# Kernel optimization log

Measured on AMD Instinct MI355X. Metric: run time of the kernel, lower is better.

The kernel has to match this reference:

```python
import jax, jax.numpy as jnp
import numpy as np

B, N, D, KD = 8, 2048, 64, 64

def setup_inputs() -> dict:
    key = jax.random.key(0)
    ks = jax.random.split(key, 7)
    s = 1.0 / np.sqrt(D)
    return {
        "x":  jax.random.normal(ks[0], (B, N, D), dtype=jnp.float32),
        "Wq": jax.random.normal(ks[1], (D, KD), dtype=jnp.float32) * s,
        "bq": jnp.zeros((KD,), jnp.float32),
        "Wk": jax.random.normal(ks[2], (D, KD), dtype=jnp.float32) * s,
        "bk": jnp.zeros((KD,), jnp.float32),
        "Wv": jax.random.normal(ks[3], (D, KD), dtype=jnp.float32) * s,
        "bv": jnp.zeros((KD,), jnp.float32),
    }

def reference(x, Wq, bq, Wk, bk, Wv, bv):
    # Q,K,V: [B,N,KD]
    Q = x @ Wq + bq
    K = x @ Wk + bk
    V = x @ Wv + bv
    # scores: [B,N,N] (note: original applies NO 1/sqrt(d) scaling)
    scores = jnp.einsum('bij,bkj->bik', Q, K)
    probs = jax.nn.softmax(scores, axis=-1)
    # mean-threshold sparsification: keep entries above the row mean
    mask = (probs > jnp.mean(probs, axis=-1, keepdims=True)).astype(probs.dtype)
    sparse = probs * mask
    out = jnp.einsum('bij,bjk->bik', sparse, V)  # [B,N,KD]
    return out
```

## Files before the change

### kernel.cpp

```cpp
#include <hip/hip_runtime.h>

#define NB 8
#define NS 2048
#define ND 64
#define LOG2E 1.44269504f

typedef _Float16 half8 __attribute__((ext_vector_type(8)));
typedef __attribute__((ext_vector_type(4))) float floatx4;

__device__ __forceinline__ half8 cvt8(const float* p) {
    float4 a = *(const float4*)p;
    float4 b = *(const float4*)(p + 4);
    half8 h = {(_Float16)a.x, (_Float16)a.y, (_Float16)a.z, (_Float16)a.w,
               (_Float16)b.x, (_Float16)b.y, (_Float16)b.z, (_Float16)b.w};
    return h;
}
__device__ __forceinline__ half8 cvtWcol(const float* base) {
    half8 h;
#pragma unroll
    for (int j = 0; j < 8; ++j) h[j] = (_Float16)base[j * 64];
    return h;
}

__global__ __launch_bounds__(256) void qkv_proj(
    const float* __restrict__ x,
    const float* __restrict__ Wq, const float* __restrict__ bq,
    const float* __restrict__ Wk, const float* __restrict__ bk,
    const float* __restrict__ Wv, const float* __restrict__ bv,
    _Float16* __restrict__ Qg, _Float16* __restrict__ Kg,
    _Float16* __restrict__ Vt)
{
    __shared__ _Float16 vt[64 * 18];

    const int tid  = threadIdx.x;
    const int wv   = tid >> 6;
    const int l    = tid & 63;
    const int quad = l >> 4;
    const int tx   = l & 15;

    const int b  = blockIdx.x & 7;
    const int n0 = (blockIdx.x >> 3) * 16;

    const float* xr = x + ((size_t)b * NS + n0 + tx) * ND + quad * 8;
    half8 a0 = cvt8(xr);
    half8 a1 = cvt8(xr + 32);

    const floatx4 zf = {0.f, 0.f, 0.f, 0.f};

#pragma unroll
    for (int i = 0; i < 3; ++i) {
        const int ct = wv * 3 + i;
        const int m  = ct >> 2;
        const int lcol = (ct & 3) * 16 + tx;

        const float* Wm;
        const float* Bm;
        if (m == 0)      { Wm = Wq; Bm = bq; }
        else if (m == 1) { Wm = Wk; Bm = bk; }
        else             { Wm = Wv; Bm = bv; }

        half8 b0 = cvtWcol(Wm + (quad * 8) * 64 + lcol);
        half8 b1 = cvtWcol(Wm + (32 + quad * 8) * 64 + lcol);

        floatx4 acc = __builtin_amdgcn_mfma_f32_16x16x32_f16(a0, b0, zf, 0, 0, 0);
        acc = __builtin_amdgcn_mfma_f32_16x16x32_f16(a1, b1, acc, 0, 0, 0);
        const float bias = Bm[lcol];

        if (m == 0) {
#pragma unroll
            for (int r = 0; r < 4; ++r)
                Qg[((size_t)b * NS + n0 + quad * 4 + r) * ND + lcol] =
                    (_Float16)((acc[r] + bias) * LOG2E);
        } else if (m == 1) {
#pragma unroll
            for (int r = 0; r < 4; ++r)
                Kg[((size_t)b * NS + n0 + quad * 4 + r) * ND + lcol] = (_Float16)(acc[r] + bias);
        } else {
#pragma unroll
            for (int r = 0; r < 4; ++r)
                vt[lcol * 18 + quad * 4 + r] = (_Float16)(acc[r] + bias);
        }
    }
    __syncthreads();
    {
        const int d = tid >> 2, seg = tid & 3;
        uint2 p = *(uint2*)&vt[d * 18 + seg * 4];
        *(uint2*)(Vt + ((size_t)b * ND + d) * NS + n0 + seg * 4) = p;
    }
}

__global__ __launch_bounds__(512, 4) void attn(
    const _Float16* __restrict__ Qg,
    const _Float16* __restrict__ Kg,
    const _Float16* __restrict__ Vt,
    float* __restrict__ out)
{
    __shared__ __align__(16) unsigned char smraw[8 * 2 * 16 * 76 * 2];
    __shared__ float lsh[128];
    _Float16* pbuf = (_Float16*)smraw;
    float*    obuf = (float*)smraw;

    const int tid  = threadIdx.x;
    const int wv   = tid >> 6;
    const int l    = tid & 63;
    const int quad = l >> 4;
    const int tx   = l & 15;

    const int b  = blockIdx.x & 7;
    const int q0 = (blockIdx.x >> 3) * 16;

    const _Float16* Qb = Qg + ((size_t)b * NS + q0) * ND;
    const _Float16* Kb = Kg + (size_t)b * NS * ND;
    const _Float16* Vb = Vt + (size_t)b * ND * NS;

    half8 qf0 = *(const half8*)(Qb + (size_t)tx * ND + quad * 8);
    half8 qf1 = *(const half8*)(Qb + (size_t)tx * ND + 32 + quad * 8);

    const floatx4 zf = {0.f, 0.f, 0.f, 0.f};

#define KROW(s) ((((s) >> 2) * 8 + wv) * 64 + ((s) & 3) * 16 + tx)

    floatx4 e[4][4];
    float lacc[4] = {0.f, 0.f, 0.f, 0.f};
    {
        half8 kf[6][2];
#pragma unroll
        for (int s = 0; s < 6; ++s) {
            const _Float16* Kr = Kb + (size_t)KROW(s) * ND + quad * 8;
            kf[s][0] = *(const half8*)Kr;
            kf[s][1] = *(const half8*)(Kr + 32);
        }
#pragma unroll
        for (int s = 0; s < 16; ++s) {
            floatx4 c = __builtin_amdgcn_mfma_f32_16x16x32_f16(qf0, kf[s % 6][0], zf, 0, 0, 0);
            c = __builtin_amdgcn_mfma_f32_16x16x32_f16(qf1, kf[s % 6][1], c, 0, 0, 0);
            if (s + 6 < 16) {
                const _Float16* Kr = Kb + (size_t)KROW(s + 6) * ND + quad * 8;
                kf[s % 6][0] = *(const half8*)Kr;
                kf[s % 6][1] = *(const half8*)(Kr + 32);
            }
#pragma unroll
            for (int r = 0; r < 4; ++r) {
                float ee = __builtin_amdgcn_exp2f(c[r]);
                e[s >> 2][s & 3][r] = ee;
                lacc[r] += ee;
            }
        }
    }
#pragma unroll
    for (int off = 1; off < 16; off <<= 1)
#pragma unroll
        for (int r = 0; r < 4; ++r)
            lacc[r] += __shfl_xor(lacc[r], off);
    if (tx == 0) {
#pragma unroll
        for (int r = 0; r < 4; ++r)
            lsh[wv * 16 + quad * 4 + r] = lacc[r];
    }

    half8 vf[4][2];
#pragma unroll
    for (int nt = 0; nt < 4; ++nt) {
        const _Float16* Vr = Vb + (size_t)(nt * 16 + tx) * NS + (0 * 8 + wv) * 64 + quad * 8;
        vf[nt][0] = *(const half8*)Vr;
        vf[nt][1] = *(const half8*)(Vr + 32);
    }
    __syncthreads();

    float inv[4], thr[4];
#pragma unroll
    for (int r = 0; r < 4; ++r) {
        const int row = quad * 4 + r;
        float L = 0.f;
#pragma unroll
        for (int w = 0; w < 8; ++w) L += lsh[w * 16 + row];
        inv[r] = 1.f / L;
        thr[r] = L * (1.f / (float)NS);
    }

    floatx4 o[4] = {zf, zf, zf, zf};
    _Float16* pb0 = pbuf + wv * (2 * 16 * 76);
    _Float16* pb1 = pb0 + 16 * 76;

#pragma unroll
    for (int nt = 0; nt < 4; ++nt)
#pragma unroll
        for (int r = 0; r < 4; ++r) {
            float ee = e[0][nt][r];
            float w = (ee > thr[r]) ? ee * inv[r] : 0.f;
            pb0[(quad * 4 + r) * 76 + nt * 16 + tx] = (_Float16)w;
        }

#pragma unroll
    for (int t = 0; t < 4; ++t) {
        _Float16* pbc = (t & 1) ? pb1 : pb0;
        _Float16* pbn = (t & 1) ? pb0 : pb1;

        half8 af0 = *(const half8*)(pbc + tx * 76 + quad * 8);
        half8 af1 = *(const half8*)(pbc + tx * 76 + 32 + quad * 8);

        if (t < 3) {
#pragma unroll
            for (int nt = 0; nt < 4; ++nt)
#pragma unroll
                for (int r = 0; r < 4; ++r) {
                    float ee = e[t + 1][nt][r];
                    float w = (ee > thr[r]) ? ee * inv[r] : 0.f;
                    pbn[(quad * 4 + r) * 76 + nt * 16 + tx] = (_Float16)w;
                }
        }

#pragma unroll
        for (int nt = 0; nt < 4; ++nt)
            o[nt] = __builtin_amdgcn_mfma_f32_16x16x32_f16(af0, vf[nt][0], o[nt], 0, 0, 0);
#pragma unroll
        for (int nt = 0; nt < 4; ++nt)
            o[nt] = __builtin_amdgcn_mfma_f32_16x16x32_f16(af1, vf[nt][1], o[nt], 0, 0, 0);

        if (t < 3) {
            const int kb = ((t + 1) * 8 + wv) * 64;
#pragma unroll
            for (int nt = 0; nt < 4; ++nt) {
                const _Float16* Vr = Vb + (size_t)(nt * 16 + tx) * NS + kb + quad * 8;
                vf[nt][0] = *(const half8*)Vr;
                vf[nt][1] = *(const half8*)(Vr + 32);
            }
        }
    }

    __syncthreads();
#pragma unroll
    for (int nt = 0; nt < 4; ++nt)
#pragma unroll
        for (int r = 0; r < 4; ++r)
            obuf[(wv * 16 + quad * 4 + r) * 68 + nt * 16 + tx] = o[nt][r];
    __syncthreads();

    {
        const int row = tid >> 5;
        const int c2  = (tid & 31) * 2;
        float sx = 0.f, sy = 0.f;
#pragma unroll
        for (int w = 0; w < 8; ++w) {
            float2 v = *(float2*)&obuf[(w * 16 + row) * 68 + c2];
            sx += v.x; sy += v.y;
        }
        float2 res = {sx, sy};
        *(float2*)(out + ((size_t)b * NS + q0 + row) * ND + c2) = res;
    }
#undef KROW
}

extern "C" void kernel_launch(void* const* d_in, const int* in_sizes, int n_in,
                              void* d_out, int out_size, void* d_ws, size_t ws_size,
                              hipStream_t stream) {
    const float* x  = (const float*)d_in[0];
    const float* Wq = (const float*)d_in[1];
    const float* bq = (const float*)d_in[2];
    const float* Wk = (const float*)d_in[3];
    const float* bk = (const float*)d_in[4];
    const float* Wv = (const float*)d_in[5];
    const float* bv = (const float*)d_in[6];

    _Float16* Qg = (_Float16*)d_ws;
    _Float16* Kg = Qg + (size_t)NB * NS * ND;
    _Float16* Vt = Kg + (size_t)NB * NS * ND;

    qkv_proj<<<NB * (NS / 16), 256, 0, stream>>>(x, Wq, bq, Wk, bk, Wv, bv, Qg, Kg, Vt);
    attn<<<NB * (NS / 16), 512, 0, stream>>>(Qg, Kg, Vt, (float*)d_out);
}
```

Before: 132.6 us.

## Pack exp scores to bf16 and shrink LDS/register footprint in attention

```diff
diff --git a/kernel.cpp b/kernel.cpp
--- a/kernel.cpp
+++ b/kernel.cpp
@@ -6,6 +6,7 @@
 #define LOG2E 1.44269504f
 
 typedef _Float16 half8 __attribute__((ext_vector_type(8)));
+typedef _Float16 half2v __attribute__((ext_vector_type(2)));
 typedef __attribute__((ext_vector_type(4))) float floatx4;
 
 __device__ __forceinline__ half8 cvt8(const float* p) {
@@ -20,6 +21,13 @@
 #pragma unroll
     for (int j = 0; j < 8; ++j) h[j] = (_Float16)base[j * 64];
     return h;
+}
+__device__ __forceinline__ unsigned f2bf(float f) {
+    unsigned u = __builtin_bit_cast(unsigned, f);
+    return (u + 0x7fffu + ((u >> 16) & 1u)) >> 16;
+}
+__device__ __forceinline__ float bf2f(unsigned lo16) {
+    return __builtin_bit_cast(float, lo16 << 16);
 }
 
 __global__ __launch_bounds__(256) void qkv_proj(
@@ -95,10 +103,10 @@
     const _Float16* __restrict__ Vt,
     float* __restrict__ out)
 {
-    __shared__ __align__(16) unsigned char smraw[8 * 2 * 16 * 76 * 2];
+    __shared__ __align__(16) unsigned char smraw[128 * 72 * 2];
     __shared__ float lsh[128];
     _Float16* pbuf = (_Float16*)smraw;
-    float*    obuf = (float*)smraw;
+    _Float16* obuf = (_Float16*)smraw;
 
     const int tid  = threadIdx.x;
     const int wv   = tid >> 6;
@@ -120,31 +128,32 @@
 
 #define KROW(s) ((((s) >> 2) * 8 + wv) * 64 + ((s) & 3) * 16 + tx)
 
-    floatx4 e[4][4];
+    unsigned e2[32];
     float lacc[4] = {0.f, 0.f, 0.f, 0.f};
     {
-        half8 kf[6][2];
-#pragma unroll
-        for (int s = 0; s < 6; ++s) {
+        half8 kf[2][2];
+#pragma unroll
+        for (int s = 0; s < 2; ++s) {
             const _Float16* Kr = Kb + (size_t)KROW(s) * ND + quad * 8;
             kf[s][0] = *(const half8*)Kr;
             kf[s][1] = *(const half8*)(Kr + 32);
         }
 #pragma unroll
         for (int s = 0; s < 16; ++s) {
-            floatx4 c = __builtin_amdgcn_mfma_f32_16x16x32_f16(qf0, kf[s % 6][0], zf, 0, 0, 0);
-            c = __builtin_amdgcn_mfma_f32_16x16x32_f16(qf1, kf[s % 6][1], c, 0, 0, 0);
-            if (s + 6 < 16) {
-                const _Float16* Kr = Kb + (size_t)KROW(s + 6) * ND + quad * 8;
-                kf[s % 6][0] = *(const half8*)Kr;
-                kf[s % 6][1] = *(const half8*)(Kr + 32);
+            floatx4 c = __builtin_amdgcn_mfma_f32_16x16x32_f16(qf0, kf[s & 1][0], zf, 0, 0, 0);
+            c = __builtin_amdgcn_mfma_f32_16x16x32_f16(qf1, kf[s & 1][1], c, 0, 0, 0);
+            if (s + 2 < 16) {
+                const _Float16* Kr = Kb + (size_t)KROW(s + 2) * ND + quad * 8;
+                kf[s & 1][0] = *(const half8*)Kr;
+                kf[s & 1][1] = *(const half8*)(Kr + 32);
             }
-#pragma unroll
-            for (int r = 0; r < 4; ++r) {
-                float ee = __builtin_amdgcn_exp2f(c[r]);
-                e[s >> 2][s & 3][r] = ee;
-                lacc[r] += ee;
-            }
+            float e0 = __builtin_amdgcn_exp2f(c[0]);
+            float e1 = __builtin_amdgcn_exp2f(c[1]);
+            float eA = __builtin_amdgcn_exp2f(c[2]);
+            float e3 = __builtin_amdgcn_exp2f(c[3]);
+            lacc[0] += e0; lacc[1] += e1; lacc[2] += eA; lacc[3] += e3;
+            e2[2 * s]     = f2bf(e0) | (f2bf(e1) << 16);
+            e2[2 * s + 1] = f2bf(eA) | (f2bf(e3) << 16);
         }
     }
 #pragma unroll
@@ -157,14 +166,6 @@
         for (int r = 0; r < 4; ++r)
             lsh[wv * 16 + quad * 4 + r] = lacc[r];
     }
-
-    half8 vf[4][2];
-#pragma unroll
-    for (int nt = 0; nt < 4; ++nt) {
-        const _Float16* Vr = Vb + (size_t)(nt * 16 + tx) * NS + (0 * 8 + wv) * 64 + quad * 8;
-        vf[nt][0] = *(const half8*)Vr;
-        vf[nt][1] = *(const half8*)(Vr + 32);
-    }
     __syncthreads();
 
     float inv[4], thr[4];
@@ -179,61 +180,40 @@
     }
 
     floatx4 o[4] = {zf, zf, zf, zf};
-    _Float16* pb0 = pbuf + wv * (2 * 16 * 76);
-    _Float16* pb1 = pb0 + 16 * 76;
-
+    _Float16* pb = pbuf + wv * (16 * 40);
+
+#pragma unroll
+    for (int c = 0; c < 8; ++c) {
+        const int vkb = ((c >> 1) * 8 + wv) * 64 + (c & 1) * 32;
+        half8 vf[4];
+#pragma unroll
+        for (int nt = 0; nt < 4; ++nt)
+            vf[nt] = *(const half8*)(Vb + (size_t)(nt * 16 + tx) * NS + vkb + quad * 8);
+
+#pragma unroll
+        for (int h = 0; h < 2; ++h) {
+            const int s = 2 * c + h;
+            unsigned u0 = e2[2 * s], u1 = e2[2 * s + 1];
+            float ev[4] = {bf2f(u0 & 0xffffu), bf2f(u0 >> 16),
+                           bf2f(u1 & 0xffffu), bf2f(u1 >> 16)};
+#pragma unroll
+            for (int r = 0; r < 4; ++r) {
+                float w = (ev[r] > thr[r]) ? ev[r] * inv[r] : 0.f;
+                pb[(quad * 4 + r) * 40 + h * 16 + tx] = (_Float16)w;
+            }
+        }
+        half8 af = *(const half8*)(pb + tx * 40 + quad * 8);
+#pragma unroll
+        for (int nt = 0; nt < 4; ++nt)
+            o[nt] = __builtin_amdgcn_mfma_f32_16x16x32_f16(af, vf[nt], o[nt], 0, 0, 0);
+    }
+
+    __syncthreads();
 #pragma unroll
     for (int nt = 0; nt < 4; ++nt)
 #pragma unroll
-        for (int r = 0; r < 4; ++r) {
-            float ee = e[0][nt][r];
-            float w = (ee > thr[r]) ? ee * inv[r] : 0.f;
-            pb0[(quad * 4 + r) * 76 + nt * 16 + tx] = (_Float16)w;
-        }
-
-#pragma unroll
-    for (int t = 0; t < 4; ++t) {
-        _Float16* pbc = (t & 1) ? pb1 : pb0;
-        _Float16* pbn = (t & 1) ? pb0 : pb1;
-
-        half8 af0 = *(const half8*)(pbc + tx * 76 + quad * 8);
-        half8 af1 = *(const half8*)(pbc + tx * 76 + 32 + quad * 8);
-
-        if (t < 3) {
-#pragma unroll
-            for (int nt = 0; nt < 4; ++nt)
-#pragma unroll
-                for (int r = 0; r < 4; ++r) {
-                    float ee = e[t + 1][nt][r];
-                    float w = (ee > thr[r]) ? ee * inv[r] : 0.f;
-                    pbn[(quad * 4 + r) * 76 + nt * 16 + tx] = (_Float16)w;
-                }
-        }
-
-#pragma unroll
-        for (int nt = 0; nt < 4; ++nt)
-            o[nt] = __builtin_amdgcn_mfma_f32_16x16x32_f16(af0, vf[nt][0], o[nt], 0, 0, 0);
-#pragma unroll
-        for (int nt = 0; nt < 4; ++nt)
-            o[nt] = __builtin_amdgcn_mfma_f32_16x16x32_f16(af1, vf[nt][1], o[nt], 0, 0, 0);
-
-        if (t < 3) {
-            const int kb = ((t + 1) * 8 + wv) * 64;
-#pragma unroll
-            for (int nt = 0; nt < 4; ++nt) {
-                const _Float16* Vr = Vb + (size_t)(nt * 16 + tx) * NS + kb + quad * 8;
-                vf[nt][0] = *(const half8*)Vr;
-                vf[nt][1] = *(const half8*)(Vr + 32);
-            }
-        }
-    }
-
-    __syncthreads();
-#pragma unroll
-    for (int nt = 0; nt < 4; ++nt)
-#pragma unroll
         for (int r = 0; r < 4; ++r)
-            obuf[(wv * 16 + quad * 4 + r) * 68 + nt * 16 + tx] = o[nt][r];
+            obuf[(wv * 16 + quad * 4 + r) * 72 + nt * 16 + tx] = (_Float16)o[nt][r];
     __syncthreads();
 
     {
@@ -242,8 +222,8 @@
         float sx = 0.f, sy = 0.f;
 #pragma unroll
         for (int w = 0; w < 8; ++w) {
-            float2 v = *(float2*)&obuf[(w * 16 + row) * 68 + c2];
-            sx += v.x; sy += v.y;
+            half2v v = *(half2v*)&obuf[(w * 16 + row) * 72 + c2];
+            sx += (float)v.x; sy += (float)v.y;
         }
         float2 res = {sx, sy};
         *(float2*)(out + ((size_t)b * NS + q0 + row) * ND + c2) = res;
```

Result: no change. 133.8 us (+0.9%).
